# Kernel tuning notes

Hardware: AMD Instinct MI355X
Metric: run time of the kernel (lower is better)

## Reference

```python
import jax, jax.numpy as jnp
import numpy as np

D_IN = 1024
D_OUT = 1024
NUM_HEADS = 16
HEAD_DIM = D_OUT // NUM_HEADS


def setup_inputs() -> dict:
    key = jax.random.key(0)
    k1, k2, k3, k4 = jax.random.split(key, 4)
    x = jax.random.normal(k1, (2, 2048, D_IN), dtype=jnp.float32)
    # qkv Linear (bias=False): weight [3*d_out, d_in]
    w_qkv = jax.random.normal(k2, (3 * D_OUT, D_IN), dtype=jnp.float32) * (1.0 / np.sqrt(D_IN))
    # proj Linear (default bias=True): weight [d_out, d_out], bias [d_out]
    w_proj = jax.random.normal(k3, (D_OUT, D_OUT), dtype=jnp.float32) * (1.0 / np.sqrt(D_OUT))
    b_proj = jax.random.normal(k4, (D_OUT,), dtype=jnp.float32) * 0.01
    return {"x": x, "w_qkv": w_qkv, "w_proj": w_proj, "b_proj": b_proj}


def reference(x, w_qkv, w_proj, b_proj):
    B, S, E = x.shape
    qkv = jnp.einsum("bse,fe->bsf", x, w_qkv)                 # [B,S,3*d_out]
    qkv = qkv.reshape(B, S, 3, NUM_HEADS, HEAD_DIM)
    qkv = jnp.transpose(qkv, (2, 0, 3, 1, 4))                  # [3,B,H,S,D]
    q, k, v = qkv[0], qkv[1], qkv[2]
    scores = jnp.einsum("bhqd,bhkd->bhqk", q, k)               # [B,H,S,S]
    causal = jnp.triu(jnp.ones((S, S), dtype=bool), k=1)
    scores = jnp.where(causal, -jnp.inf, scores)
    # NOTE: source divides by head_dim**(-0.5), i.e. multiplies by sqrt(head_dim)
    scores = scores / (HEAD_DIM ** -0.5)
    attn = jax.nn.softmax(scores, axis=-1)
    ctx = jnp.einsum("bhqk,bhkd->bhqd", attn, v)               # [B,H,S,D]
    ctx = jnp.transpose(ctx, (0, 2, 1, 3)).reshape(B, S, E)
    return jnp.einsum("bse,fe->bsf", ctx, w_proj) + b_proj
```

## Files before the change

kernel.cpp:

```cpp
#include <hip/hip_runtime.h>

typedef _Float16 f16;
typedef _Float16 f16x4 __attribute__((ext_vector_type(4)));
typedef _Float16 f16x8 __attribute__((ext_vector_type(8)));
typedef float f32x4 __attribute__((ext_vector_type(4)));

#define MFMA16(a, b, c) __builtin_amdgcn_mfma_f32_16x16x32_f16(a, b, c, 0, 0, 0)
#define QSCALE 11.5415603f

typedef const __attribute__((address_space(1))) void* gp1_t;
typedef __attribute__((address_space(3))) void* lp3_t;
__device__ __forceinline__ void gld16(const void* g, void* l) {
    __builtin_amdgcn_global_load_lds((gp1_t)g, (lp3_t)l, 16, 0, 0);
}

__global__ __launch_bounds__(256) void cvt_all(
    const float* __restrict__ x, const float* __restrict__ wq, const float* __restrict__ wp,
    f16* __restrict__ xh, f16* __restrict__ wqh, f16* __restrict__ wph)
{
    int i = blockIdx.x * 256 + threadIdx.x;
    const float4* src; f16x4* dst; int off;
    if (i < 1048576)      { src = (const float4*)x;  dst = (f16x4*)xh;  off = i; }
    else if (i < 1835008) { src = (const float4*)wq; dst = (f16x4*)wqh; off = i - 1048576; }
    else                  { src = (const float4*)wp; dst = (f16x4*)wph; off = i - 1835008; }
    float4 v = src[off];
    f16x4 o = { (f16)v.x, (f16)v.y, (f16)v.z, (f16)v.w };
    dst[off] = o;
}

template<int EPI>
__global__ __launch_bounds__(256) void gemm_k(
    const f16* __restrict__ A, const f16* __restrict__ B, int K,
    f16* __restrict__ qb, f16* __restrict__ kb, f16* __restrict__ vt,
    float* __restrict__ outF, const float* __restrict__ bias)
{
    __shared__ f16 as[128 * 32];
    __shared__ f16 bs[128 * 32];
    const int t = threadIdx.x;
    const int m0 = blockIdx.y * 128, n0 = blockIdx.x * 128;
    const int lane = t & 63, wv = t >> 6;
    const int wm = wv >> 1, wn = wv & 1;
    const int lr = lane & 15, g = lane >> 4;
    const int srow = lane >> 2, schk = (lane & 3) * 8;
    const f16* Ab = A + (size_t)m0 * K;
    const f16* Bb = B + (size_t)n0 * K;
    f32x4 acc[4][4] = {};

    for (int k0 = 0; k0 < K; k0 += 32) {
        __syncthreads();
        #pragma unroll
        for (int i2 = 0; i2 < 2; ++i2) {
            const int r0 = wv * 32 + i2 * 16;
            gld16(&Ab[(size_t)(r0 + srow) * K + k0 + schk], &as[r0 * 32]);
            gld16(&Bb[(size_t)(r0 + srow) * K + k0 + schk], &bs[r0 * 32]);
        }
        __syncthreads();
        f16x8 af[4], bf[4];
        #pragma unroll
        for (int mt = 0; mt < 4; ++mt)
            af[mt] = *reinterpret_cast<const f16x8*>(&as[(wm * 64 + mt * 16 + lr) * 32 + g * 8]);
        #pragma unroll
        for (int nt = 0; nt < 4; ++nt)
            bf[nt] = *reinterpret_cast<const f16x8*>(&bs[(wn * 64 + nt * 16 + lr) * 32 + g * 8]);
        #pragma unroll
        for (int mt = 0; mt < 4; ++mt)
            #pragma unroll
            for (int nt = 0; nt < 4; ++nt)
                acc[mt][nt] = MFMA16(af[mt], bf[nt], acc[mt][nt]);
    }

    #pragma unroll
    for (int mt = 0; mt < 4; ++mt) {
        #pragma unroll
        for (int nt = 0; nt < 4; ++nt) {
            const int n = n0 + wn * 64 + nt * 16 + lr;
            const int s0 = m0 + wm * 64 + mt * 16 + 4 * g;
            if (EPI == 0) {
                const int which = n >> 10, h = (n >> 6) & 15, d = n & 63;
                const int b = s0 >> 11, s = s0 & 2047;
                if (which == 2) {
                    f16x4 vv;
                    #pragma unroll
                    for (int i = 0; i < 4; ++i) vv[i] = (f16)acc[mt][nt][i];
                    *reinterpret_cast<f16x4*>(&vt[((size_t)((b << 4) + h) * 64 + d) * 2048 + s]) = vv;
                } else {
                    f16* dst = which ? kb : qb;
                    const float sc = which ? 1.0f : QSCALE;
                    #pragma unroll
                    for (int i = 0; i < 4; ++i)
                        dst[((size_t)((b << 4) + h) * 2048 + (s + i)) * 64 + d] = (f16)(acc[mt][nt][i] * sc);
                }
            } else {
                #pragma unroll
                for (int i = 0; i < 4; ++i)
                    outF[(size_t)(s0 + i) * 1024 + n] = acc[mt][nt][i] + bias[n];
            }
        }
    }
}

__global__ __launch_bounds__(64, 2) void attn_k(
    const f16* __restrict__ Q, const f16* __restrict__ K, const f16* __restrict__ VT,
    f16* __restrict__ ctx, f16* __restrict__ opart,
    float* __restrict__ mpart, float* __restrict__ lpart)
{
    __shared__ f16 lp[64][72];
    const int lane = threadIdx.x;
    const int lr = lane & 15, g = lane >> 4;
    const int bid = blockIdx.x;
    const int bh = bid & 31;
    const int rr = 67 - (bid >> 5);
    int u, c;
    if (rr < 10)      { u = rr;                 c = 0; }
    else if (rr < 30) { u = 10 + (rr - 10) / 2; c = (rr - 10) % 2; }
    else if (rr < 60) { u = 20 + (rr - 30) / 3; c = (rr - 30) % 3; }
    else              { u = 30 + (rr - 60) / 4; c = (rr - 60) % 4; }
    const int ntt = u + 1;
    const int nc  = 1 + u / 10;
    const int cbase = ntt / nc, crem = ntt % nc;
    const int start = c * cbase + (c < crem ? c : crem);
    const int len   = cbase + (c < crem ? 1 : 0);
    const bool diag = (start + len == ntt);

    const int b = bh >> 4, h = bh & 15;
    const size_t base = (size_t)bh * (2048 * 64);
    const f16* Qb = Q + base;
    const f16* Kb = K + base;
    const f16* Vb = VT + base;
    const int q0 = u << 6;

    f16x8 qf[4][2];
    #pragma unroll
    for (int nt = 0; nt < 4; ++nt)
        #pragma unroll
        for (int ks = 0; ks < 2; ++ks)
            qf[nt][ks] = *reinterpret_cast<const f16x8*>(&Qb[(size_t)(q0 + nt * 16 + lr) * 64 + ks * 32 + g * 8]);

    f32x4 o[4][4] = {};
    float mrun[4] = { -1e30f, -1e30f, -1e30f, -1e30f };
    float lsum[4] = { 0.f, 0.f, 0.f, 0.f };

#define ATTN_TILE(KV0, DIAGM) do {                                                      \
    const int kv0_ = (KV0);                                                             \
    f32x4 st[4][4] = {};                                                                \
    _Pragma("unroll")                                                                   \
    for (int mt = 0; mt < 4; ++mt) {                                                    \
        f16x8 ak[2];                                                                    \
        _Pragma("unroll")                                                               \
        for (int ks = 0; ks < 2; ++ks)                                                  \
            ak[ks] = *reinterpret_cast<const f16x8*>(                                   \
                &Kb[(size_t)(kv0_ + mt * 16 + lr) * 64 + ks * 32 + g * 8]);             \
        _Pragma("unroll")                                                               \
        for (int nt = 0; nt < 4; ++nt)                                                  \
            if (!(DIAGM) || mt <= nt) {                                                 \
                _Pragma("unroll")                                                       \
                for (int ks = 0; ks < 2; ++ks)                                          \
                    st[mt][nt] = MFMA16(ak[ks], qf[nt][ks], st[mt][nt]);                \
            }                                                                           \
    }                                                                                   \
    _Pragma("unroll")                                                                   \
    for (int nt = 0; nt < 4; ++nt) {                                                    \
        float mloc = -1e30f;                                                            \
        _Pragma("unroll")                                                               \
        for (int mt = 0; mt < 4; ++mt) {                                                \
            if ((DIAGM) && mt > nt) continue;                                           \
            _Pragma("unroll")                                                           \
            for (int i = 0; i < 4; ++i) {                                               \
                float sv = st[mt][nt][i];                                               \
                if ((DIAGM) && mt == nt) {             \
                    sv = (4 * g + i <= lr) ? sv : -1e30f;                               \
                    st[mt][nt][i] = sv;                                                 \
                }                                                                       \
                mloc = fmaxf(mloc, sv);                                                 \
            }                                                                           \
        }                                                                               \
        mloc = fmaxf(mloc, __shfl_xor(mloc, 16));                                       \
        mloc = fmaxf(mloc, __shfl_xor(mloc, 32));                                       \
        if (__any(mloc > mrun[nt] + 8.0f)) {                             \
            float mnew = fmaxf(mrun[nt], mloc);                                         \
            float sc = exp2f(mrun[nt] - mnew);                                          \
            lsum[nt] *= sc;                                                             \
            _Pragma("unroll")                                                           \
            for (int mo = 0; mo < 4; ++mo)                                              \
                _Pragma("unroll")                                                       \
                for (int i = 0; i < 4; ++i) o[mo][nt][i] *= sc;                         \
            mrun[nt] = mnew;                                                            \
        }                                                                               \
        float ls = 0.f;                                                                 \
        _Pragma("unroll")                                                               \
        for (int mt = 0; mt < 4; ++mt) {                                                \
            f16x4 pk;                                                                   \
            if ((DIAGM) && mt > nt) {                                                   \
                pk[0] = pk[1] = pk[2] = pk[3] = (f16)0.f;                               \
            } else {                                                                    \
                _Pragma("unroll")                                                       \
                for (int i = 0; i < 4; ++i) {                                           \
                    float p = exp2f(st[mt][nt][i] - mrun[nt]);                          \
                    ls += p; pk[i] = (f16)p;                                            \
                }                                                                       \
            }                                                                           \
            *reinterpret_cast<f16x4*>(&lp[nt * 16 + lr][mt * 16 + 4 * g]) = pk;         \
        }                                                                               \
        lsum[nt] += ls;                                                                 \
    }                                                                                   \
    {                                                                                   \
        f16x8 pf[4][2];                                                                 \
        _Pragma("unroll")                                                               \
        for (int nt = 0; nt < 4; ++nt)                                                  \
            _Pragma("unroll")                                                           \
            for (int ks = 0; ks < 2; ++ks)                                              \
                pf[nt][ks] = *reinterpret_cast<const f16x8*>(                           \
                    &lp[nt * 16 + lr][ks * 32 + g * 8]);                                \
        _Pragma("unroll")                                                               \
        for (int mo = 0; mo < 4; ++mo) {                                                \
            f16x8 av[2];                                                                \
            _Pragma("unroll")                                                           \
            for (int ks = 0; ks < 2; ++ks)                                              \
                av[ks] = *reinterpret_cast<const f16x8*>(                               \
                    &Vb[(size_t)(mo * 16 + lr) * 2048 + kv0_ + ks * 32 + g * 8]);       \
            _Pragma("unroll")                                                           \
            for (int nt = 0; nt < 4; ++nt)                                              \
                _Pragma("unroll")                                                       \
                for (int ks = 0; ks < 2; ++ks)                                          \
                    o[mo][nt] = MFMA16(av[ks], pf[nt][ks], o[mo][nt]);                  \
        }                                                                               \
    }                                                                                   \
} while (0)

    const int tEnd = start + len - (diag ? 1 : 0);
    for (int tt = start; tt < tEnd; ++tt)
        ATTN_TILE(tt << 6, 0);
    if (diag)
        ATTN_TILE((ntt - 1) << 6, 1);
#undef ATTN_TILE

    const bool split = (nc > 1);
    int slot = 0;
    if (split) {
        const int psl = (u < 20) ? 2 * (u - 10) : (u < 30 ? 20 + 3 * (u - 20) : 50 + 4 * (u - 30));
        slot = bh * 58 + psl + c;
    }
    #pragma unroll
    for (int nt = 0; nt < 4; ++nt) {
        float l = lsum[nt];
        l += __shfl_xor(l, 16);
        l += __shfl_xor(l, 32);
        const float inv = 1.0f / l;
        const int lrow = nt * 16 + lr;
        if (!split) {
            const size_t rowoff = ((size_t)(b * 2048 + q0 + lrow)) * 1024 + h * 64;
            #pragma unroll
            for (int mo = 0; mo < 4; ++mo) {
                f16x4 ov;
                #pragma unroll
                for (int i = 0; i < 4; ++i) ov[i] = (f16)(o[mo][nt][i] * inv);
                *reinterpret_cast<f16x4*>(&ctx[rowoff + mo * 16 + 4 * g]) = ov;
            }
        } else {
            const int mi = slot * 64 + lrow;
            #pragma unroll
            for (int mo = 0; mo < 4; ++mo) {
                f16x4 ov;
                #pragma unroll
                for (int i = 0; i < 4; ++i) ov[i] = (f16)(o[mo][nt][i] * inv);
                *reinterpret_cast<f16x4*>(&opart[(size_t)mi * 64 + mo * 16 + 4 * g]) = ov;
            }
            if (g == 0) { mpart[mi] = mrun[nt]; lpart[mi] = l; }
        }
    }
}

__global__ __launch_bounds__(256) void combine_k(
    const f16* __restrict__ opart, const float* __restrict__ mpart,
    const float* __restrict__ lpart, f16* __restrict__ ctx)
{
    const int blk = blockIdx.x;
    const int bh = blk & 31, u = 10 + (blk >> 5);
    const int b = bh >> 4, h = bh & 15;
    const int nc = 1 + u / 10;
    const int psl = (u < 20) ? 2 * (u - 10) : (u < 30 ? 20 + 3 * (u - 20) : 50 + 4 * (u - 30));
    const int slot0 = bh * 58 + psl;
    const int t = threadIdx.x;
    const int lrow = t >> 2, seg = t & 3;

    float m[4], l[4], w[4];
    float M = -1e30f;
    #pragma unroll 4
    for (int cc = 0; cc < 4; ++cc) if (cc < nc) {
        m[cc] = mpart[(slot0 + cc) * 64 + lrow];
        l[cc] = lpart[(slot0 + cc) * 64 + lrow];
        M = fmaxf(M, m[cc]);
    }
    float wsum = 0.f;
    #pragma unroll 4
    for (int cc = 0; cc < 4; ++cc) if (cc < nc) { w[cc] = l[cc] * exp2f(m[cc] - M); wsum += w[cc]; }
    const float r = 1.0f / wsum;

    float acc[16] = {};
    #pragma unroll 4
    for (int cc = 0; cc < 4; ++cc) if (cc < nc) {
        const float coef = w[cc] * r;
        const size_t rb = (size_t)((slot0 + cc) * 64 + lrow) * 64 + seg * 16;
        f16x8 v0 = *reinterpret_cast<const f16x8*>(&opart[rb]);
        f16x8 v1 = *reinterpret_cast<const f16x8*>(&opart[rb + 8]);
        #pragma unroll
        for (int i = 0; i < 8; ++i) { acc[i] += coef * (float)v0[i]; acc[i + 8] += coef * (float)v1[i]; }
    }
    f16x8 o0, o1;
    #pragma unroll
    for (int i = 0; i < 8; ++i) { o0[i] = (f16)acc[i]; o1[i] = (f16)acc[i + 8]; }
    const size_t wb = ((size_t)(b * 2048 + u * 64 + lrow)) * 1024 + h * 64 + seg * 16;
    *reinterpret_cast<f16x8*>(&ctx[wb]) = o0;
    *reinterpret_cast<f16x8*>(&ctx[wb + 8]) = o1;
}

extern "C" void kernel_launch(void* const* d_in, const int* in_sizes, int n_in,
                              void* d_out, int out_size, void* d_ws, size_t ws_size,
                              hipStream_t stream) {
    const float* x      = (const float*)d_in[0];
    const float* w_qkv  = (const float*)d_in[1];
    const float* w_proj = (const float*)d_in[2];
    const float* b_proj = (const float*)d_in[3];
    float* out = (float*)d_out;

    char* p = (char*)d_ws;
    f16* xh     = (f16*)p; p += (size_t)4096 * 1024 * 2;
    f16* wqkvh  = (f16*)p; p += (size_t)3072 * 1024 * 2;
    f16* wprojh = (f16*)p; p += (size_t)1024 * 1024 * 2;
    f16* qbuf   = (f16*)p; p += (size_t)2 * 16 * 2048 * 64 * 2;
    f16* kbuf   = (f16*)p; p += (size_t)2 * 16 * 2048 * 64 * 2;
    f16* vtbuf  = (f16*)p; p += (size_t)2 * 16 * 64 * 2048 * 2;
    f16* ctx    = (f16*)p; p += (size_t)4096 * 1024 * 2;

    f16*   opart = (f16*)d_out;
    float* mpart = (float*)xh;
    float* lpart = mpart + 118784;

    cvt_all<<<8192, 256, 0, stream>>>(x, w_qkv, w_proj, xh, wqkvh, wprojh);

    gemm_k<0><<<dim3(24, 32), 256, 0, stream>>>(xh, wqkvh, 1024, qbuf, kbuf, vtbuf, nullptr, nullptr);

    attn_k<<<2176, 64, 0, stream>>>(qbuf, kbuf, vtbuf, ctx, opart, mpart, lpart);

    combine_k<<<704, 256, 0, stream>>>(opart, mpart, lpart, ctx);

    gemm_k<1><<<dim3(8, 32), 256, 0, stream>>>(ctx, wprojh, 1024, nullptr, nullptr, nullptr, out, b_proj);
}
```

Before: 199.5 us.

## Split attention rows into more KV chunks, swizzle GEMM blocks, narrow proj tiles

Attention query tiles of index 10 and up are now split into roughly (u+5)/5 KV chunks, up to 7, instead of 1+u/10. This raises the block count from 2176 to 3648 so long causal rows spread across more CUs. Partial outputs are spread over three reused scratch regions, and the combine kernel merges up to 7 partials. The GEMM gains a block-index swizzle meant to improve L2 locality, and the projection GEMM uses 128x64 tiles to double its block count. In exchange there is more partial-output traffic and combine work, and smaller projection tiles reuse less data per block.

```diff
diff --git a/kernel.cpp b/kernel.cpp
--- a/kernel.cpp
+++ b/kernel.cpp
@@ -12,6 +12,14 @@
 typedef __attribute__((address_space(3))) void* lp3_t;
 __device__ __forceinline__ void gld16(const void* g, void* l) {
     __builtin_amdgcn_global_load_lds((gp1_t)g, (lp3_t)l, 16, 0, 0);
+}
+
+__device__ __forceinline__ int unit_psl(int u) {
+    return (u < 15) ? 3 * (u - 10)
+         : (u < 20) ? 15 + 4 * (u - 15)
+         : (u < 25) ? 35 + 5 * (u - 20)
+         : (u < 30) ? 60 + 6 * (u - 25)
+         :            90 + 7 * (u - 30);
 }
 
 __global__ __launch_bounds__(256) void cvt_all(
@@ -28,23 +36,28 @@
     dst[off] = o;
 }
 
-template<int EPI>
+template<int EPI, int BN>
 __global__ __launch_bounds__(256) void gemm_k(
     const f16* __restrict__ A, const f16* __restrict__ B, int K,
     f16* __restrict__ qb, f16* __restrict__ kb, f16* __restrict__ vt,
     float* __restrict__ outF, const float* __restrict__ bias)
 {
     __shared__ f16 as[128 * 32];
-    __shared__ f16 bs[128 * 32];
+    __shared__ f16 bs[BN * 32];
+    constexpr int WN = BN / 2;
+    constexpr int NT = BN / 32;
     const int t = threadIdx.x;
-    const int m0 = blockIdx.y * 128, n0 = blockIdx.x * 128;
+    const int bidf = blockIdx.y * gridDim.x + blockIdx.x;
+    const int cpx  = (gridDim.x * gridDim.y) >> 3;
+    const int swz  = (bidf & 7) * cpx + (bidf >> 3);
+    const int m0 = (swz / gridDim.x) * 128, n0 = (swz % gridDim.x) * BN;
     const int lane = t & 63, wv = t >> 6;
     const int wm = wv >> 1, wn = wv & 1;
     const int lr = lane & 15, g = lane >> 4;
     const int srow = lane >> 2, schk = (lane & 3) * 8;
     const f16* Ab = A + (size_t)m0 * K;
     const f16* Bb = B + (size_t)n0 * K;
-    f32x4 acc[4][4] = {};
+    f32x4 acc[4][NT] = {};
 
     for (int k0 = 0; k0 < K; k0 += 32) {
         __syncthreads();
@@ -52,28 +65,37 @@
         for (int i2 = 0; i2 < 2; ++i2) {
             const int r0 = wv * 32 + i2 * 16;
             gld16(&Ab[(size_t)(r0 + srow) * K + k0 + schk], &as[r0 * 32]);
+        }
+        if constexpr (BN == 128) {
+            #pragma unroll
+            for (int i2 = 0; i2 < 2; ++i2) {
+                const int r0 = wv * 32 + i2 * 16;
+                gld16(&Bb[(size_t)(r0 + srow) * K + k0 + schk], &bs[r0 * 32]);
+            }
+        } else {
+            const int r0 = wv * 16;
             gld16(&Bb[(size_t)(r0 + srow) * K + k0 + schk], &bs[r0 * 32]);
         }
         __syncthreads();
-        f16x8 af[4], bf[4];
+        f16x8 af[4], bf[NT];
         #pragma unroll
         for (int mt = 0; mt < 4; ++mt)
             af[mt] = *reinterpret_cast<const f16x8*>(&as[(wm * 64 + mt * 16 + lr) * 32 + g * 8]);
         #pragma unroll
-        for (int nt = 0; nt < 4; ++nt)
-            bf[nt] = *reinterpret_cast<const f16x8*>(&bs[(wn * 64 + nt * 16 + lr) * 32 + g * 8]);
+        for (int nt = 0; nt < NT; ++nt)
+            bf[nt] = *reinterpret_cast<const f16x8*>(&bs[(wn * WN + nt * 16 + lr) * 32 + g * 8]);
         #pragma unroll
         for (int mt = 0; mt < 4; ++mt)
             #pragma unroll
-            for (int nt = 0; nt < 4; ++nt)
+            for (int nt = 0; nt < NT; ++nt)
                 acc[mt][nt] = MFMA16(af[mt], bf[nt], acc[mt][nt]);
     }
 
     #pragma unroll
     for (int mt = 0; mt < 4; ++mt) {
         #pragma unroll
-        for (int nt = 0; nt < 4; ++nt) {
-            const int n = n0 + wn * 64 + nt * 16 + lr;
+        for (int nt = 0; nt < NT; ++nt) {
+            const int n = n0 + wn * WN + nt * 16 + lr;
             const int s0 = m0 + wm * 64 + mt * 16 + 4 * g;
             if (EPI == 0) {
                 const int which = n >> 10, h = (n >> 6) & 15, d = n & 63;
@@ -101,7 +123,7 @@
 
 __global__ __launch_bounds__(64, 2) void attn_k(
     const f16* __restrict__ Q, const f16* __restrict__ K, const f16* __restrict__ VT,
-    f16* __restrict__ ctx, f16* __restrict__ opart,
+    f16* __restrict__ ctx, f16* __restrict__ op0, f16* __restrict__ op1, f16* __restrict__ op2,
     float* __restrict__ mpart, float* __restrict__ lpart)
 {
     __shared__ f16 lp[64][72];
@@ -109,14 +131,16 @@
     const int lr = lane & 15, g = lane >> 4;
     const int bid = blockIdx.x;
     const int bh = bid & 31;
-    const int rr = 67 - (bid >> 5);
+    const int rest = bid >> 5;
     int u, c;
-    if (rr < 10)      { u = rr;                 c = 0; }
-    else if (rr < 30) { u = 10 + (rr - 10) / 2; c = (rr - 10) % 2; }
-    else if (rr < 60) { u = 20 + (rr - 30) / 3; c = (rr - 30) % 3; }
-    else              { u = 30 + (rr - 60) / 4; c = (rr - 60) % 4; }
+    if (rest < 14)       { u = 31 - rest / 7;          c = rest % 7; }
+    else if (rest < 44)  { u = 29 - (rest - 14) / 6;   c = (rest - 14) % 6; }
+    else if (rest < 69)  { u = 24 - (rest - 44) / 5;   c = (rest - 44) % 5; }
+    else if (rest < 89)  { u = 19 - (rest - 69) / 4;   c = (rest - 69) % 4; }
+    else if (rest < 104) { u = 14 - (rest - 89) / 3;   c = (rest - 89) % 3; }
+    else                 { u = 9 - (rest - 104);       c = 0; }
     const int ntt = u + 1;
-    const int nc  = 1 + u / 10;
+    const int nc  = (u < 10) ? 1 : (u + 5) / 5;
     const int cbase = ntt / nc, crem = ntt % nc;
     const int start = c * cbase + (c < crem ? c : crem);
     const int len   = cbase + (c < crem ? 1 : 0);
@@ -234,11 +258,13 @@
         ATTN_TILE((ntt - 1) << 6, 1);
 #undef ATTN_TILE
 
-    const bool split = (nc > 1);
-    int slot = 0;
+    const bool split = (u >= 10);
+    f16* osl = nullptr; int G = 0;
     if (split) {
-        const int psl = (u < 20) ? 2 * (u - 10) : (u < 30 ? 20 + 3 * (u - 20) : 50 + 4 * (u - 30));
-        slot = bh * 58 + psl + c;
+        G = bh * 104 + unit_psl(u) + c;
+        osl = (G < 2048) ? op0 + (size_t)G * 4096
+            : (G < 2816) ? op1 + (size_t)(G - 2048) * 4096
+            :              op2 + (size_t)(G - 2816) * 4096;
     }
     #pragma unroll
     for (int nt = 0; nt < 4; ++nt) {
@@ -253,56 +279,57 @@
             for (int mo = 0; mo < 4; ++mo) {
                 f16x4 ov;
                 #pragma unroll
-                for (int i = 0; i < 4; ++i) ov[i] = (f16)(o[mo][nt][i] * inv);
+                for (int i2 = 0; i2 < 4; ++i2) ov[i2] = (f16)(o[mo][nt][i2] * inv);
                 *reinterpret_cast<f16x4*>(&ctx[rowoff + mo * 16 + 4 * g]) = ov;
             }
         } else {
-            const int mi = slot * 64 + lrow;
             #pragma unroll
             for (int mo = 0; mo < 4; ++mo) {
                 f16x4 ov;
                 #pragma unroll
-                for (int i = 0; i < 4; ++i) ov[i] = (f16)(o[mo][nt][i] * inv);
-                *reinterpret_cast<f16x4*>(&opart[(size_t)mi * 64 + mo * 16 + 4 * g]) = ov;
+                for (int i2 = 0; i2 < 4; ++i2) ov[i2] = (f16)(o[mo][nt][i2] * inv);
+                *reinterpret_cast<f16x4*>(&osl[lrow * 64 + mo * 16 + 4 * g]) = ov;
             }
-            if (g == 0) { mpart[mi] = mrun[nt]; lpart[mi] = l; }
+            if (g == 0) { mpart[G * 64 + lrow] = mrun[nt]; lpart[G * 64 + lrow] = l; }
         }
     }
 }
 
 __global__ __launch_bounds__(256) void combine_k(
-    const f16* __restrict__ opart, const float* __restrict__ mpart,
-    const float* __restrict__ lpart, f16* __restrict__ ctx)
+    const f16* __restrict__ op0, const f16* __restrict__ op1, const f16* __restrict__ op2,
+    const float* __restrict__ mpart, const float* __restrict__ lpart, f16* __restrict__ ctx)
 {
     const int blk = blockIdx.x;
     const int bh = blk & 31, u = 10 + (blk >> 5);
     const int b = bh >> 4, h = bh & 15;
-    const int nc = 1 + u / 10;
-    const int psl = (u < 20) ? 2 * (u - 10) : (u < 30 ? 20 + 3 * (u - 20) : 50 + 4 * (u - 30));
-    const int slot0 = bh * 58 + psl;
+    const int nc = (u + 5) / 5;
+    const int G0 = bh * 104 + unit_psl(u);
     const int t = threadIdx.x;
     const int lrow = t >> 2, seg = t & 3;
 
-    float m[4], l[4], w[4];
+    float m[7], l[7], w[7];
     float M = -1e30f;
-    #pragma unroll 4
-    for (int cc = 0; cc < 4; ++cc) if (cc < nc) {
-        m[cc] = mpart[(slot0 + cc) * 64 + lrow];
-        l[cc] = lpart[(slot0 + cc) * 64 + lrow];
+    #pragma unroll
+    for (int cc = 0; cc < 7; ++cc) if (cc < nc) {
+        m[cc] = mpart[(G0 + cc) * 64 + lrow];
+        l[cc] = lpart[(G0 + cc) * 64 + lrow];
         M = fmaxf(M, m[cc]);
     }
     float wsum = 0.f;
-    #pragma unroll 4
-    for (int cc = 0; cc < 4; ++cc) if (cc < nc) { w[cc] = l[cc] * exp2f(m[cc] - M); wsum += w[cc]; }
+    #pragma unroll
+    for (int cc = 0; cc < 7; ++cc) if (cc < nc) { w[cc] = l[cc] * exp2f(m[cc] - M); wsum += w[cc]; }
     const float r = 1.0f / wsum;
 
     float acc[16] = {};
-    #pragma unroll 4
-    for (int cc = 0; cc < 4; ++cc) if (cc < nc) {
+    #pragma unroll
+    for (int cc = 0; cc < 7; ++cc) if (cc < nc) {
+        const int G = G0 + cc;
+        const f16* osl = (G < 2048) ? op0 + (size_t)G * 4096
+                       : (G < 2816) ? op1 + (size_t)(G - 2048) * 4096
+                       :              op2 + (size_t)(G - 2816) * 4096;
         const float coef = w[cc] * r;
-        const size_t rb = (size_t)((slot0 + cc) * 64 + lrow) * 64 + seg * 16;
-        f16x8 v0 = *reinterpret_cast<const f16x8*>(&opart[rb]);
-        f16x8 v1 = *reinterpret_cast<const f16x8*>(&opart[rb + 8]);
+        f16x8 v0 = *reinterpret_cast<const f16x8*>(&osl[lrow * 64 + seg * 16]);
+        f16x8 v1 = *reinterpret_cast<const f16x8*>(&osl[lrow * 64 + seg * 16 + 8]);
         #pragma unroll
         for (int i = 0; i < 8; ++i) { acc[i] += coef * (float)v0[i]; acc[i + 8] += coef * (float)v1[i]; }
     }
@@ -332,17 +359,19 @@
     f16* vtbuf  = (f16*)p; p += (size_t)2 * 16 * 64 * 2048 * 2;
     f16* ctx    = (f16*)p; p += (size_t)4096 * 1024 * 2;
 
-    f16*   opart = (f16*)d_out;
-    float* mpart = (float*)xh;
-    float* lpart = mpart + 118784;
+    f16*   op0 = (f16*)d_out;
+    f16*   op1 = wqkvh;
+    f16*   op2 = xh;
+    float* mpart = (float*)(xh + (size_t)3145728);
+    float* lpart = mpart + 212992;
 
     cvt_all<<<8192, 256, 0, stream>>>(x, w_qkv, w_proj, xh, wqkvh, wprojh);
 
-    gemm_k<0><<<dim3(24, 32), 256, 0, stream>>>(xh, wqkvh, 1024, qbuf, kbuf, vtbuf, nullptr, nullptr);
-
-    attn_k<<<2176, 64, 0, stream>>>(qbuf, kbuf, vtbuf, ctx, opart, mpart, lpart);
-
-    combine_k<<<704, 256, 0, stream>>>(opart, mpart, lpart, ctx);
-
-    gemm_k<1><<<dim3(8, 32), 256, 0, stream>>>(ctx, wprojh, 1024, nullptr, nullptr, nullptr, out, b_proj);
-}
+    gemm_k<0, 128><<<dim3(24, 32), 256, 0, stream>>>(xh, wqkvh, 1024, qbuf, kbuf, vtbuf, nullptr, nullptr);
+
+    attn_k<<<3648, 64, 0, stream>>>(qbuf, kbuf, vtbuf, ctx, op0, op1, op2, mpart, lpart);
+
+    combine_k<<<704, 256, 0, stream>>>(op0, op1, op2, mpart, lpart, ctx);
+
+    gemm_k<1, 64><<<dim3(16, 32), 256, 0, stream>>>(ctx, wprojh, 1024, nullptr, nullptr, nullptr, out, b_proj);
+}
```

After: 210.1 us. 1.05x slower.
